# Performance work log

Hardware: AMD Instinct MI355X
Metric: run time of the kernel (lower is better)

## Reference

```python
import jax, jax.numpy as jnp
import numpy as np

CODEBOOK_SIZE = 8192
TOKEN_SIZE = 256
COMMITMENT_COST = 0.25


def setup_inputs() -> dict:
    key = jax.random.key(0)
    k1, k2 = jax.random.split(key)
    z = jax.random.normal(k1, (32, 1024, TOKEN_SIZE), dtype=jnp.float32)
    # embedding initialized uniform in [-1/K, 1/K] as in torch module
    embedding = jax.random.uniform(
        k2, (CODEBOOK_SIZE, TOKEN_SIZE), dtype=jnp.float32,
        minval=-1.0 / CODEBOOK_SIZE, maxval=1.0 / CODEBOOK_SIZE)
    return {"z": z, "embedding": embedding}


def reference(z, embedding):
    B, T, D = z.shape
    zf = z.reshape(B * T, D)                               # [N, D]
    # squared euclidean distances: ||z||^2 + ||e||^2 - 2 z.e
    d = (jnp.sum(zf * zf, axis=1, keepdims=True)
         + jnp.sum(embedding * embedding, axis=1)
         - 2.0 * jnp.einsum('nd,kd->nk', zf, embedding))   # [N, K]
    idx = jnp.argmin(d, axis=1)                            # [N]
    z_q = embedding[idx].reshape(B, T, D)                  # codebook gather
    commitment_loss = COMMITMENT_COST * jnp.mean(
        (jax.lax.stop_gradient(z_q) - z) ** 2)
    codebook_loss = jnp.mean((z_q - jax.lax.stop_gradient(z)) ** 2)
    loss = commitment_loss + codebook_loss                 # ema_update=False
    # straight-through estimator
    z_q_st = z + jax.lax.stop_gradient(z_q - z)
    return (z_q_st, loss, commitment_loss, codebook_loss,
            idx.reshape(B, T))
```

## Files before the change

### kernel.cpp

```cpp
#include <hip/hip_runtime.h>
#include <hip/hip_bf16.h>
#include <cfloat>

#define N_TOK   32768
#define K_CODES 8192
#define D_DIM   256
#define BTOK    128
#define CHUNK   128
#define NSPLIT  4
#define SPLITK  (K_CODES / NSPLIT)
#define CTAU_M  3.0e-5f
#define CAND_MM 2.4e-5f
#define MAXCAND 16
#define RBTOK   32
#define NRS     8
#define RSPLIT  (K_CODES / NRS)

typedef __attribute__((ext_vector_type(4)))  short bf16x4;
typedef __attribute__((ext_vector_type(8)))  short bf16x8;
typedef __attribute__((ext_vector_type(16))) float f32x16;


__device__ __forceinline__ float np_sumsq256(const float* __restrict__ row) {
    #pragma clang fp contract(off)
    float blk[2];
    #pragma unroll
    for (int b = 0; b < 2; b++) {
        const float* x = row + b * 128;
        float r[8];
        #pragma unroll
        for (int j = 0; j < 8; j++) { float v = x[j]; r[j] = v * v; }
        for (int i = 8; i < 128; i += 8) {
            #pragma unroll
            for (int j = 0; j < 8; j++) { float v = x[i + j]; r[j] += v * v; }
        }
        blk[b] = ((r[0] + r[1]) + (r[2] + r[3])) + ((r[4] + r[5]) + (r[6] + r[7]));
    }
    return blk[0] + blk[1];
}

__device__ __forceinline__ float np_einsum256(const float* __restrict__ a,
                                              const float* __restrict__ b) {
    #pragma clang fp contract(off)
    float A0 = 0.f, A1 = 0.f, A2 = 0.f, A3 = 0.f;
    for (int m = 0; m < 256; m += 16) {
        A0 = a[m+ 0]*b[m+ 0] + (a[m+ 4]*b[m+ 4] + (a[m+ 8]*b[m+ 8] + (a[m+12]*b[m+12] + A0)));
        A1 = a[m+ 1]*b[m+ 1] + (a[m+ 5]*b[m+ 5] + (a[m+ 9]*b[m+ 9] + (a[m+13]*b[m+13] + A1)));
        A2 = a[m+ 2]*b[m+ 2] + (a[m+ 6]*b[m+ 6] + (a[m+10]*b[m+10] + (a[m+14]*b[m+14] + A2)));
        A3 = a[m+ 3]*b[m+ 3] + (a[m+ 7]*b[m+ 7] + (a[m+11]*b[m+11] + (a[m+15]*b[m+15] + A3)));
    }
    return (A0 + A1) + (A2 + A3);
}

__device__ __forceinline__ float np_dtilde(float Cn, float e2k, float g) {
    #pragma clang fp contract(off)
    float t = Cn + e2k;
    float d = t - 2.0f * g;
    return d;
}

__device__ __forceinline__ unsigned short bf16_rne(float f) {
    unsigned u = __float_as_uint(f);
    unsigned r = u + 0x7fffu + ((u >> 16) & 1u);
    return (unsigned short)(r >> 16);
}
__device__ __forceinline__ void split_bf16(float f, short& hi, short& lo) {
    unsigned short h = bf16_rne(f);
    hi = (short)h;
    float hf = __uint_as_float(((unsigned)h) << 16);
    lo = (short)bf16_rne(f - hf);
}
__device__ __forceinline__ bf16x8 lo8(bf16x8 h, float4 a, float4 b) {
    float f[8] = {a.x, a.y, a.z, a.w, b.x, b.y, b.z, b.w};
    bf16x8 r;
    #pragma unroll
    for (int i = 0; i < 8; i += 2) {
        float d0 = f[i]     - __uint_as_float(((unsigned)(unsigned short)h[i])     << 16);
        float d1 = f[i + 1] - __uint_as_float(((unsigned)(unsigned short)h[i + 1]) << 16);
        __hip_bfloat162 p = __float22bfloat162_rn(make_float2(d0, d1));
        unsigned u; __builtin_memcpy(&u, &p, 4);
        r[i]     = (short)(u & 0xffffu);
        r[i + 1] = (short)(u >> 16);
    }
    return r;
}

#define MFMA3(A, ah, al, bh, bl) \
    A = __builtin_amdgcn_mfma_f32_32x32x16_bf16(ah, bh, A, 0, 0, 0); \
    A = __builtin_amdgcn_mfma_f32_32x32x16_bf16(ah, bl, A, 0, 0, 0); \
    A = __builtin_amdgcn_mfma_f32_32x32x16_bf16(al, bh, A, 0, 0, 0);

__global__ __launch_bounds__(256) void prep_e_kernel(
    const float* __restrict__ emb, float* __restrict__ e2np,
    float* __restrict__ e2h, unsigned* __restrict__ ccount,
    double* __restrict__ loss_sum)
{
    int k = blockIdx.x * 256 + threadIdx.x;
    float v = np_sumsq256(emb + (size_t)k * D_DIM);
    e2np[k] = v;
    e2h[k]  = 0.5f * v;
    if (k == 0) { *ccount = 0u; *loss_sum = 0.0; }
}

__global__ __launch_bounds__(256) void prep_z_kernel(
    const float* __restrict__ z, float* __restrict__ Cnp)
{
    int t = blockIdx.x * 256 + threadIdx.x;
    Cnp[t] = np_sumsq256(z + (size_t)t * D_DIM);
}

__global__ __launch_bounds__(256) void cvt_e_kernel(
    const float* __restrict__ src, short* __restrict__ hi, short* __restrict__ lo)
{
    size_t p = ((size_t)blockIdx.x * 256 + threadIdx.x) * 8;
    float4 v0 = *(const float4*)(src + p);
    float4 v1 = *(const float4*)(src + p + 4);
    short h[8], l[8];
    split_bf16(v0.x, h[0], l[0]); split_bf16(v0.y, h[1], l[1]);
    split_bf16(v0.z, h[2], l[2]); split_bf16(v0.w, h[3], l[3]);
    split_bf16(v1.x, h[4], l[4]); split_bf16(v1.y, h[5], l[5]);
    split_bf16(v1.z, h[6], l[6]); split_bf16(v1.w, h[7], l[7]);
    bf16x8 vh = {h[0],h[1],h[2],h[3],h[4],h[5],h[6],h[7]};
    bf16x8 vl = {l[0],l[1],l[2],l[3],l[4],l[5],l[6],l[7]};
    *(bf16x8*)(hi + p) = vh;
    *(bf16x8*)(lo + p) = vl;
}

__global__ __launch_bounds__(256) void cvt_zhi_kernel(
    const float* __restrict__ src, short* __restrict__ hi)
{
    size_t p = ((size_t)blockIdx.x * 256 + threadIdx.x) * 8;
    float4 v0 = *(const float4*)(src + p);
    float4 v1 = *(const float4*)(src + p + 4);
    bf16x8 vh = {(short)bf16_rne(v0.x), (short)bf16_rne(v0.y),
                 (short)bf16_rne(v0.z), (short)bf16_rne(v0.w),
                 (short)bf16_rne(v1.x), (short)bf16_rne(v1.y),
                 (short)bf16_rne(v1.z), (short)bf16_rne(v1.w)};
    *(bf16x8*)(hi + p) = vh;
}

#define B_ESH 0
#define B_ESL 4096
#define B_ZSH 8192
#define B_ZSL 12288
#define TILE1 1024

__global__ __launch_bounds__(256, 2) void bulk_kernel(
    const float* __restrict__ zf, const short* __restrict__ zhi,
    const short* __restrict__ ehi, const short* __restrict__ elo,
    const float* __restrict__ e2h,
    float* __restrict__ m1a, float* __restrict__ m2a, int* __restrict__ i1a)
{
    __shared__ __align__(16) short smem[2][16384];
    __shared__ float e2s[2][CHUNK];
    __shared__ float s1m[BTOK], s2m[BTOK];
    __shared__ int   i1m[BTOK];

    const int tid  = threadIdx.x;
    const int lane = tid & 63;
    const int w    = tid >> 6;
    const int wt   = w & 1, wc = w >> 1;
    const int g     = blockIdx.x & 255;
    const int split = blockIdx.x >> 8;
    const int tok0  = g * BTOK;
    const int cs0   = split * SPLITK;

    const int r0 = tid >> 2, q0 = tid & 3;
    const int r1 = r0 + 64;
    const int so0 = r0 * 32 + ((q0 ^ ((r0 >> 1) & 3)) << 3);
    const int so1 = r1 * 32 + ((q0 ^ ((r1 >> 1) & 3)) << 3);

    const int l31 = lane & 31, hh = lane >> 5;
    const int swz = (l31 >> 1) & 3;
    const int arow = (wc * 64 + l31) * 32;
    const int brow = (wt * 64 + l31) * 32;
    const int a0 = arow + ((hh ^ swz) << 3);
    const int a1 = arow + (((2 + hh) ^ swz) << 3);
    const int b0 = brow + ((hh ^ swz) << 3);
    const int b1 = brow + (((2 + hh) ^ swz) << 3);

    float m1[2] = {-FLT_MAX, -FLT_MAX}, m2[2] = {-FLT_MAX, -FLT_MAX};
    int   k1[2] = {0x7fffffff, 0x7fffffff};

    bf16x8 eh0p, el0p, eh1p, el1p, zh0p, zh1p;
    float4 zf0ap, zf0bp, zf1ap, zf1bp;
    float  e2vp = 0.f;

    f32x16 acc[2][2];
    #pragma unroll
    for (int i = 0; i < 2; i++)
        #pragma unroll
        for (int j = 0; j < 2; j++)
            #pragma unroll
            for (int r = 0; r < 16; r++) acc[i][j][r] = 0.f;

    const int NST = (SPLITK / CHUNK) * 8;

    auto ISSUE = [&](int s) {
        const int c  = s >> 3;
        const int st = s & 7;
        const int code0 = cs0 + c * CHUNK;
        const int d0 = st * 32;
        const size_t ei0 = ((size_t)(code0 + r0) << 8) + d0 + (q0 << 3);
        const size_t ei1 = ((size_t)(code0 + r1) << 8) + d0 + (q0 << 3);
        const size_t zi0 = ((size_t)(tok0 + r0) << 8) + d0 + (q0 << 3);
        const size_t zi1 = ((size_t)(tok0 + r1) << 8) + d0 + (q0 << 3);
        eh0p = *(const bf16x8*)(ehi + ei0);
        el0p = *(const bf16x8*)(elo + ei0);
        eh1p = *(const bf16x8*)(ehi + ei1);
        el1p = *(const bf16x8*)(elo + ei1);
        zh0p = *(const bf16x8*)(zhi + zi0);
        zh1p = *(const bf16x8*)(zhi + zi1);
        zf0ap = *(const float4*)(zf + zi0);
        zf0bp = *(const float4*)(zf + zi0 + 4);
        zf1ap = *(const float4*)(zf + zi1);
        zf1bp = *(const float4*)(zf + zi1 + 4);
        if (st == 0 && tid < CHUNK) e2vp = e2h[code0 + tid];
    };

    auto STORE = [&](int buf, int s) {
        bf16x8 zl0 = lo8(zh0p, zf0ap, zf0bp);
        bf16x8 zl1 = lo8(zh1p, zf1ap, zf1bp);
        short* sm = smem[buf];
        *(bf16x8*)(sm + B_ESH + so0) = eh0p;
        *(bf16x8*)(sm + B_ESL + so0) = el0p;
        *(bf16x8*)(sm + B_ESH + so1) = eh1p;
        *(bf16x8*)(sm + B_ESL + so1) = el1p;
        *(bf16x8*)(sm + B_ZSH + so0) = zh0p;
        *(bf16x8*)(sm + B_ZSL + so0) = zl0;
        *(bf16x8*)(sm + B_ZSH + so1) = zh1p;
        *(bf16x8*)(sm + B_ZSL + so1) = zl1;
        if ((s & 7) == 0 && tid < CHUNK) e2s[(s >> 3) & 1][tid] = e2vp;
    };

    ISSUE(0);
    STORE(0, 0);
    __syncthreads();

    #pragma unroll 2
    for (int s = 0; s < NST; s++) {
        const int cur = s & 1;
        if (s + 1 < NST) ISSUE(s + 1);
        {
            const short* sm = smem[cur];
            {
                bf16x8 a0h = *(const bf16x8*)(sm + B_ESH + a0);
                bf16x8 a0l = *(const bf16x8*)(sm + B_ESL + a0);
                bf16x8 a1h = *(const bf16x8*)(sm + B_ESH + TILE1 + a0);
                bf16x8 a1l = *(const bf16x8*)(sm + B_ESL + TILE1 + a0);
                bf16x8 b0h = *(const bf16x8*)(sm + B_ZSH + b0);
                bf16x8 b0l = *(const bf16x8*)(sm + B_ZSL + b0);
                bf16x8 b1h = *(const bf16x8*)(sm + B_ZSH + TILE1 + b0);
                bf16x8 b1l = *(const bf16x8*)(sm + B_ZSL + TILE1 + b0);
                MFMA3(acc[0][0], a0h, a0l, b0h, b0l);
                MFMA3(acc[0][1], a0h, a0l, b1h, b1l);
                MFMA3(acc[1][0], a1h, a1l, b0h, b0l);
                MFMA3(acc[1][1], a1h, a1l, b1h, b1l);
            }
            {
                bf16x8 a0h = *(const bf16x8*)(sm + B_ESH + a1);
                bf16x8 a0l = *(const bf16x8*)(sm + B_ESL + a1);
                bf16x8 a1h = *(const bf16x8*)(sm + B_ESH + TILE1 + a1);
                bf16x8 a1l = *(const bf16x8*)(sm + B_ESL + TILE1 + a1);
                bf16x8 b0h = *(const bf16x8*)(sm + B_ZSH + b1);
                bf16x8 b0l = *(const bf16x8*)(sm + B_ZSL + b1);
                bf16x8 b1h = *(const bf16x8*)(sm + B_ZSH + TILE1 + b1);
                bf16x8 b1l = *(const bf16x8*)(sm + B_ZSL + TILE1 + b1);
                MFMA3(acc[0][0], a0h, a0l, b0h, b0l);
                MFMA3(acc[0][1], a0h, a0l, b1h, b1l);
                MFMA3(acc[1][0], a1h, a1l, b0h, b0l);
                MFMA3(acc[1][1], a1h, a1l, b1h, b1l);
            }
        }
        if ((s & 7) == 7) {
            const int code0 = cs0 + (s >> 3) * CHUNK;
            const float* e2c = e2s[(s >> 3) & 1];
            #pragma unroll
            for (int tc = 0; tc < 2; tc++) {
                float ev[16];
                #pragma unroll
                for (int r = 0; r < 16; r++)
                    ev[r] = e2c[wc * 64 + tc * 32 + hh * 4 + (r & 3) + ((r >> 2) << 3)];
                #pragma unroll
                for (int tt = 0; tt < 2; tt++) {
                    #pragma unroll
                    for (int r = 0; r < 16; r++) {
                        float a = acc[tc][tt][r] - ev[r];
                        int code = code0 + wc * 64 + tc * 32 + hh * 4 + (r & 3) + ((r >> 2) << 3);
                        if (a > m1[tt]) { m2[tt] = m1[tt]; m1[tt] = a; k1[tt] = code; }
                        else if (a > m2[tt]) m2[tt] = a;
                    }
                }
            }
            #pragma unroll
            for (int i = 0; i < 2; i++)
                #pragma unroll
                for (int j = 0; j < 2; j++)
                    #pragma unroll
                    for (int r = 0; r < 16; r++) acc[i][j][r] = 0.f;
        }
        if (s + 1 < NST) STORE(cur ^ 1, s + 1);
        __syncthreads();
    }

    #pragma unroll
    for (int tt = 0; tt < 2; tt++) {
        float o1 = __shfl_xor(m1[tt], 32);
        float o2 = __shfl_xor(m2[tt], 32);
        int   oi = __shfl_xor(k1[tt], 32);
        bool take = (o1 > m1[tt]) || (o1 == m1[tt] && oi < k1[tt]);
        float w1 = take ? o1 : m1[tt];
        int   wi = take ? oi : k1[tt];
        float ls = take ? m1[tt] : o1;
        m2[tt] = fmaxf(fmaxf(m2[tt], o2), ls);
        m1[tt] = w1; k1[tt] = wi;
    }
    __syncthreads();
    if (wc == 0 && lane < 32) {
        #pragma unroll
        for (int tt = 0; tt < 2; tt++) {
            int tl = wt * 64 + tt * 32 + lane;
            s1m[tl] = m1[tt]; s2m[tl] = m2[tt]; i1m[tl] = k1[tt];
        }
    }
    __syncthreads();
    if (wc == 1 && lane < 32) {
        #pragma unroll
        for (int tt = 0; tt < 2; tt++) {
            int tl = wt * 64 + tt * 32 + lane;
            float a1 = s1m[tl], a2 = s2m[tl]; int ai = i1m[tl];
            bool take = (a1 > m1[tt]) || (a1 == m1[tt] && ai < k1[tt]);
            float w1 = take ? a1 : m1[tt];
            int   wi = take ? ai : k1[tt];
            float ls = take ? m1[tt] : a1;
            float w2 = fmaxf(fmaxf(m2[tt], a2), ls);
            size_t t = (size_t)(tok0 + tl) * NSPLIT + split;
            m1a[t] = w1; m2a[t] = w2; i1a[t] = wi;
        }
    }
}

__global__ __launch_bounds__(256) void merge_kernel(
    const float* __restrict__ m1a, const float* __restrict__ m2a,
    const int* __restrict__ i1a, float* __restrict__ m1f,
    int* __restrict__ idxf, int* __restrict__ clist,
    unsigned* __restrict__ ccount, unsigned* __restrict__ ccnt_g)
{
    int t = blockIdx.x * 256 + threadIdx.x;
    ccnt_g[t] = 0u;
    float w1 = m1a[t * NSPLIT], w2 = m2a[t * NSPLIT];
    int   wi = i1a[t * NSPLIT];
    #pragma unroll
    for (int s = 1; s < NSPLIT; s++) {
        float a1 = m1a[t * NSPLIT + s], a2 = m2a[t * NSPLIT + s];
        int   ai = i1a[t * NSPLIT + s];
        bool take = (a1 > w1) || (a1 == w1 && ai < wi);
        float n1 = take ? a1 : w1;
        int   ni = take ? ai : wi;
        float ls = take ? w1 : a1;
        w2 = fmaxf(fmaxf(w2, a2), ls);
        w1 = n1; wi = ni;
    }
    idxf[t] = wi; m1f[t] = w1;
    if (w1 - w2 < CTAU_M) {
        unsigned p = atomicAdd(ccount, 1u);
        clist[p] = t;
    }
}

#define R_ESH 0
#define R_ESL 4096
#define R_ZSH 8192
#define R_ZSL 9216

__global__ __launch_bounds__(256) void rescue_kernel(
    const float* __restrict__ zf, const short* __restrict__ zhi,
    const short* __restrict__ ehi, const short* __restrict__ elo,
    const float* __restrict__ e2h, const float* __restrict__ m1f,
    const unsigned* __restrict__ ccount, const int* __restrict__ clist,
    unsigned* __restrict__ ccnt_g, int* __restrict__ cand_g)
{
    const unsigned count = *ccount;
    const unsigned base  = blockIdx.x * RBTOK;
    if (base >= count) return;
    const int nt = min(RBTOK, (int)(count - base));
    const int sp = blockIdx.y;

    __shared__ __align__(16) short rsm[10240];
    __shared__ int   tls[RBTOK];
    __shared__ float thr[RBTOK];
    __shared__ float e2s[CHUNK];

    const int tid  = threadIdx.x;
    const int lane = tid & 63;
    const int w    = tid >> 6;

    if (tid < RBTOK) {
        int s = (tid < nt) ? tid : (nt - 1);
        int t = clist[base + s];
        tls[tid] = t;
        thr[tid] = (tid < nt) ? (m1f[t] - CAND_MM) : FLT_MAX;
    }
    __syncthreads();

    const int l31 = lane & 31, hh = lane >> 5;
    const float mythr = thr[l31];
    const int   mytok = tls[l31];
    const int swz = (l31 >> 1) & 3;
    const int arow = (w * 32 + l31) * 32;
    const int brow = l31 * 32;
    const int a0 = arow + ((hh ^ swz) << 3);
    const int a1 = arow + (((2 + hh) ^ swz) << 3);
    const int b0 = brow + ((hh ^ swz) << 3);
    const int b1 = brow + (((2 + hh) ^ swz) << 3);

    const int er0 = tid >> 2, eq0 = tid & 3;
    const int er1 = er0 + 64;
    const int eso0 = er0 * 32 + ((eq0 ^ ((er0 >> 1) & 3)) << 3);
    const int eso1 = er1 * 32 + ((eq0 ^ ((er1 >> 1) & 3)) << 3);
    const int zr = (tid & 127) >> 2, zq = tid & 3;
    const int zso = zr * 32 + ((zq ^ ((zr >> 1) & 3)) << 3);

    for (int c = 0; c < RSPLIT / CHUNK; c++) {
        const int code0 = sp * RSPLIT + c * CHUNK;
        const float e2v = (tid < CHUNK) ? e2h[code0 + tid] : 0.f;
        f32x16 acc;
        #pragma unroll
        for (int r = 0; r < 16; r++) acc[r] = 0.f;

        for (int st = 0; st < 8; st++) {
            const int d0 = st * 32;
            const size_t ei0 = ((size_t)(code0 + er0) << 8) + d0 + (eq0 << 3);
            const size_t ei1 = ((size_t)(code0 + er1) << 8) + d0 + (eq0 << 3);
            bf16x8 eh0 = *(const bf16x8*)(ehi + ei0);
            bf16x8 el0 = *(const bf16x8*)(elo + ei0);
            bf16x8 eh1 = *(const bf16x8*)(ehi + ei1);
            bf16x8 el1 = *(const bf16x8*)(elo + ei1);
            bf16x8 zh = {}, zl = {};
            if (tid < 128) {
                const size_t zi = ((size_t)tls[zr] << 8) + d0 + (zq << 3);
                zh = *(const bf16x8*)(zhi + zi);
                float4 za = *(const float4*)(zf + zi);
                float4 zb = *(const float4*)(zf + zi + 4);
                zl = lo8(zh, za, zb);
            }
            __syncthreads();
            *(bf16x8*)(rsm + R_ESH + eso0) = eh0;
            *(bf16x8*)(rsm + R_ESL + eso0) = el0;
            *(bf16x8*)(rsm + R_ESH + eso1) = eh1;
            *(bf16x8*)(rsm + R_ESL + eso1) = el1;
            if (tid < 128) {
                *(bf16x8*)(rsm + R_ZSH + zso) = zh;
                *(bf16x8*)(rsm + R_ZSL + zso) = zl;
            }
            if (st == 0 && tid < CHUNK) e2s[tid] = e2v;
            __syncthreads();
            {
                bf16x8 ah = *(const bf16x8*)(rsm + R_ESH + a0);
                bf16x8 al = *(const bf16x8*)(rsm + R_ESL + a0);
                bf16x8 bh = *(const bf16x8*)(rsm + R_ZSH + b0);
                bf16x8 bl = *(const bf16x8*)(rsm + R_ZSL + b0);
                MFMA3(acc, ah, al, bh, bl);
            }
            {
                bf16x8 ah = *(const bf16x8*)(rsm + R_ESH + a1);
                bf16x8 al = *(const bf16x8*)(rsm + R_ESL + a1);
                bf16x8 bh = *(const bf16x8*)(rsm + R_ZSH + b1);
                bf16x8 bl = *(const bf16x8*)(rsm + R_ZSL + b1);
                MFMA3(acc, ah, al, bh, bl);
            }
        }
        #pragma unroll
        for (int r = 0; r < 16; r++) {
            const int local = w * 32 + hh * 4 + (r & 3) + ((r >> 2) << 3);
            float a = acc[r] - e2s[local];
            if (a >= mythr) {
                unsigned p = atomicAdd(&ccnt_g[mytok], 1u);
                if (p < MAXCAND) cand_g[(size_t)mytok * MAXCAND + p] = code0 + local;
            }
        }
    }
}

__global__ __launch_bounds__(256) void resolve_kernel(
    const float* __restrict__ z, const float* __restrict__ emb,
    const float* __restrict__ e2np, const float* __restrict__ Cnp,
    const unsigned* __restrict__ ccount, const int* __restrict__ clist,
    const unsigned* __restrict__ ccnt_g, const int* __restrict__ cand_g,
    int* __restrict__ idxf)
{
    const unsigned count = *ccount;
    const int lane = threadIdx.x & 63;
    const int w    = threadIdx.x >> 6;
    for (unsigned c = blockIdx.x * 4 + w; c < count; c += gridDim.x * 4) {
        const int t = clist[c];
        const int n = (int)min(ccnt_g[t], (unsigned)MAXCAND);
        float bd = FLT_MAX; int bk = 0x7fffffff;
        if (lane < n) {
            const int k = cand_g[(size_t)t * MAXCAND + lane];
            float g = np_einsum256(z + (size_t)t * D_DIM, emb + (size_t)k * D_DIM);
            bd = np_dtilde(Cnp[t], e2np[k], g);
            bk = k;
        }
        #pragma unroll
        for (int off = 32; off >= 1; off >>= 1) {
            float od = __shfl_xor(bd, off);
            int   ok = __shfl_xor(bk, off);
            if (od < bd || (od == bd && ok < bk)) { bd = od; bk = ok; }
        }
        if (lane == 0 && n > 0) idxf[t] = bk;
    }
}

__global__ __launch_bounds__(256) void out_loss_kernel(
    const float* __restrict__ z, const float* __restrict__ emb,
    const int* __restrict__ idxf, float* __restrict__ out0,
    double* __restrict__ loss_sum)
{
    const int total4 = N_TOK * (D_DIM / 4);
    double lsum = 0.0;
    for (int p = blockIdx.x * 256 + threadIdx.x; p < total4; p += gridDim.x * 256) {
        const int n  = p >> 6;
        const int d4 = p & 63;
        const int k  = idxf[n];
        float4 zv = ((const float4*)z)[p];
        float4 ev = ((const float4*)(emb + (size_t)k * D_DIM))[d4];
        float dx = ev.x - zv.x, dy = ev.y - zv.y,
              dz = ev.z - zv.z, dw = ev.w - zv.w;
        float4 o;
        o.x = zv.x + dx; o.y = zv.y + dy; o.z = zv.z + dz; o.w = zv.w + dw;
        ((float4*)out0)[p] = o;
        lsum += (double)dx * dx + (double)dy * dy
              + (double)dz * dz + (double)dw * dw;
    }
    #pragma unroll
    for (int off = 32; off >= 1; off >>= 1) lsum += __shfl_xor(lsum, off);
    __shared__ double wsum[4];
    const int wv = threadIdx.x >> 6;
    if ((threadIdx.x & 63) == 0) wsum[wv] = lsum;
    __syncthreads();
    if (threadIdx.x == 0)
        atomicAdd(loss_sum, wsum[0] + wsum[1] + wsum[2] + wsum[3]);
}

__global__ __launch_bounds__(256) void finalize_kernel(
    const int* __restrict__ idxf, const double* __restrict__ loss_sum,
    float* __restrict__ out)
{
    const int t = blockIdx.x * 256 + threadIdx.x;
    if (t < N_TOK) out[8388611 + t] = (float)idxf[t];
    if (t == 0) {
        double mse = *loss_sum * (1.0 / 8388608.0);
        out[8388608] = (float)(1.25 * mse);
        out[8388609] = (float)(0.25 * mse);
        out[8388610] = (float)mse;
    }
}

extern "C" void kernel_launch(void* const* d_in, const int* in_sizes, int n_in,
                              void* d_out, int out_size, void* d_ws, size_t ws_size,
                              hipStream_t stream)
{
    const float* z   = (const float*)d_in[0];
    const float* emb = (const float*)d_in[1];
    float* out = (float*)d_out;
    char*  ws  = (char*)d_ws;
    char*  ob  = (char*)d_out;

    short*    ehi    = (short*)(ob + 0);
    short*    elo    = (short*)(ob + 4194304);
    short*    zhi    = (short*)(ob + 8388608);
    float*    m1a    = (float*)(ob + 25165824);
    float*    m2a    = (float*)(ob + 25690112);
    int*      i1a    = (int*)(ob + 26214400);
    int*      cand_g = (int*)(ob + 26738688);

    double*   loss_sum = (double*)(ws + 0);
    unsigned* ccount   = (unsigned*)(ws + 8);
    float*    e2np     = (float*)(ws + 16);
    float*    e2h      = (float*)(ws + 32784);
    float*    Cnp      = (float*)(ws + 65552);
    float*    m1f      = (float*)(ws + 196624);
    int*      idxf     = (int*)(ws + 327696);
    int*      clist    = (int*)(ws + 458768);
    unsigned* ccnt_g   = (unsigned*)(ws + 589840);

    prep_e_kernel<<<dim3(K_CODES / 256), dim3(256), 0, stream>>>(
        emb, e2np, e2h, ccount, loss_sum);
    prep_z_kernel<<<dim3(N_TOK / 256), dim3(256), 0, stream>>>(z, Cnp);
    cvt_e_kernel<<<dim3(K_CODES * D_DIM / 8 / 256), dim3(256), 0, stream>>>(emb, ehi, elo);
    cvt_zhi_kernel<<<dim3(N_TOK * D_DIM / 8 / 256), dim3(256), 0, stream>>>(z, zhi);
    bulk_kernel<<<dim3((N_TOK / BTOK) * NSPLIT), dim3(256), 0, stream>>>(
        z, zhi, ehi, elo, e2h, m1a, m2a, i1a);
    merge_kernel<<<dim3(N_TOK / 256), dim3(256), 0, stream>>>(
        m1a, m2a, i1a, m1f, idxf, clist, ccount, ccnt_g);
    rescue_kernel<<<dim3(N_TOK / RBTOK, NRS), dim3(256), 0, stream>>>(
        z, zhi, ehi, elo, e2h, m1f, ccount, clist, ccnt_g, cand_g);
    resolve_kernel<<<dim3(128), dim3(256), 0, stream>>>(
        z, emb, e2np, Cnp, ccount, clist, ccnt_g, cand_g, idxf);
    out_loss_kernel<<<dim3(1024), dim3(256), 0, stream>>>(
        z, emb, idxf, out, loss_sum);
    finalize_kernel<<<dim3(N_TOK / 256), dim3(256), 0, stream>>>(
        idxf, loss_sum, out);
}
```

Before: 802.0 us.

## Load bf16 tiles directly into LDS via global_load_lds, recompute z hi/lo split

The main distance kernel now copies the embedding hi/lo and z hi bf16 tiles straight from global memory into shared memory with the global_load_lds builtin. Before, they were staged through registers and written with ds_write. The XOR swizzle moves into the global address so each lane's LDS destination stays contiguous. The z low part is now computed from the fp32 z alone by a new split helper, so the zhi register copy is no longer needed. This cuts VGPR pressure and LDS store instructions, but the asynchronous writes go into the other buffer while the current one is read, so correctness depends on the existing barrier and vmcnt ordering.

```diff
diff --git a/kernel.cpp b/kernel.cpp
--- a/kernel.cpp
+++ b/kernel.cpp
@@ -84,6 +84,26 @@
     }
     return r;
 }
+__device__ __forceinline__ uint4 zsplit8(float4 a, float4 b) {
+    float f[8] = {a.x, a.y, a.z, a.w, b.x, b.y, b.z, b.w};
+    unsigned u[4];
+    #pragma unroll
+    for (int i = 0; i < 4; i++) {
+        __hip_bfloat162 hp = __float22bfloat162_rn(make_float2(f[2*i], f[2*i+1]));
+        unsigned hu; __builtin_memcpy(&hu, &hp, 4);
+        float h0 = __uint_as_float(hu << 16);
+        float h1 = __uint_as_float(hu & 0xffff0000u);
+        __hip_bfloat162 lp = __float22bfloat162_rn(make_float2(f[2*i] - h0, f[2*i+1] - h1));
+        __builtin_memcpy(&u[i], &lp, 4);
+    }
+    return make_uint4(u[0], u[1], u[2], u[3]);
+}
+
+__device__ __forceinline__ void gl_lds16(const short* g, short* l) {
+    __builtin_amdgcn_global_load_lds(
+        (const __attribute__((address_space(1))) void*)g,
+        (__attribute__((address_space(3))) void*)l, 16, 0, 0);
+}
 
 #define MFMA3(A, ah, al, bh, bl) \
     A = __builtin_amdgcn_mfma_f32_32x32x16_bf16(ah, bh, A, 0, 0, 0); \
@@ -167,8 +187,12 @@
 
     const int r0 = tid >> 2, q0 = tid & 3;
     const int r1 = r0 + 64;
-    const int so0 = r0 * 32 + ((q0 ^ ((r0 >> 1) & 3)) << 3);
-    const int so1 = r1 * 32 + ((q0 ^ ((r1 >> 1) & 3)) << 3);
+    const int swz0 = (r0 >> 1) & 3;
+    const int qs   = q0 ^ swz0;
+    const int so0 = r0 * 32 + (qs << 3);
+    const int so1 = r1 * 32 + (qs << 3);
+    const int dls0 = w * 512;
+    const int dls1 = w * 512 + 2048;
 
     const int l31 = lane & 31, hh = lane >> 5;
     const int swz = (l31 >> 1) & 3;
@@ -182,7 +206,6 @@
     float m1[2] = {-FLT_MAX, -FLT_MAX}, m2[2] = {-FLT_MAX, -FLT_MAX};
     int   k1[2] = {0x7fffffff, 0x7fffffff};
 
-    bf16x8 eh0p, el0p, eh1p, el1p, zh0p, zh1p;
     float4 zf0ap, zf0bp, zf1ap, zf1bp;
     float  e2vp = 0.f;
 
@@ -196,21 +219,24 @@
 
     const int NST = (SPLITK / CHUNK) * 8;
 
-    auto ISSUE = [&](int s) {
+    auto ISSUE = [&](int s, int buf) {
         const int c  = s >> 3;
         const int st = s & 7;
         const int code0 = cs0 + c * CHUNK;
         const int d0 = st * 32;
-        const size_t ei0 = ((size_t)(code0 + r0) << 8) + d0 + (q0 << 3);
-        const size_t ei1 = ((size_t)(code0 + r1) << 8) + d0 + (q0 << 3);
+        short* sm = smem[buf];
+        const size_t eg0 = ((size_t)(code0 + r0) << 8) + d0 + (qs << 3);
+        const size_t eg1 = ((size_t)(code0 + r1) << 8) + d0 + (qs << 3);
+        const size_t zg0 = ((size_t)(tok0 + r0) << 8) + d0 + (qs << 3);
+        const size_t zg1 = ((size_t)(tok0 + r1) << 8) + d0 + (qs << 3);
+        gl_lds16(ehi + eg0, sm + B_ESH + dls0);
+        gl_lds16(ehi + eg1, sm + B_ESH + dls1);
+        gl_lds16(elo + eg0, sm + B_ESL + dls0);
+        gl_lds16(elo + eg1, sm + B_ESL + dls1);
+        gl_lds16(zhi + zg0, sm + B_ZSH + dls0);
+        gl_lds16(zhi + zg1, sm + B_ZSH + dls1);
         const size_t zi0 = ((size_t)(tok0 + r0) << 8) + d0 + (q0 << 3);
         const size_t zi1 = ((size_t)(tok0 + r1) << 8) + d0 + (q0 << 3);
-        eh0p = *(const bf16x8*)(ehi + ei0);
-        el0p = *(const bf16x8*)(elo + ei0);
-        eh1p = *(const bf16x8*)(ehi + ei1);
-        el1p = *(const bf16x8*)(elo + ei1);
-        zh0p = *(const bf16x8*)(zhi + zi0);
-        zh1p = *(const bf16x8*)(zhi + zi1);
         zf0ap = *(const float4*)(zf + zi0);
         zf0bp = *(const float4*)(zf + zi0 + 4);
         zf1ap = *(const float4*)(zf + zi1);
@@ -219,28 +245,22 @@
     };
 
     auto STORE = [&](int buf, int s) {
-        bf16x8 zl0 = lo8(zh0p, zf0ap, zf0bp);
-        bf16x8 zl1 = lo8(zh1p, zf1ap, zf1bp);
+        uint4 zl0 = zsplit8(zf0ap, zf0bp);
+        uint4 zl1 = zsplit8(zf1ap, zf1bp);
         short* sm = smem[buf];
-        *(bf16x8*)(sm + B_ESH + so0) = eh0p;
-        *(bf16x8*)(sm + B_ESL + so0) = el0p;
-        *(bf16x8*)(sm + B_ESH + so1) = eh1p;
-        *(bf16x8*)(sm + B_ESL + so1) = el1p;
-        *(bf16x8*)(sm + B_ZSH + so0) = zh0p;
-        *(bf16x8*)(sm + B_ZSL + so0) = zl0;
-        *(bf16x8*)(sm + B_ZSH + so1) = zh1p;
-        *(bf16x8*)(sm + B_ZSL + so1) = zl1;
+        *(uint4*)(sm + B_ZSL + so0) = zl0;
+        *(uint4*)(sm + B_ZSL + so1) = zl1;
         if ((s & 7) == 0 && tid < CHUNK) e2s[(s >> 3) & 1][tid] = e2vp;
     };
 
-    ISSUE(0);
+    ISSUE(0, 0);
     STORE(0, 0);
     __syncthreads();
 
     #pragma unroll 2
     for (int s = 0; s < NST; s++) {
         const int cur = s & 1;
-        if (s + 1 < NST) ISSUE(s + 1);
+        if (s + 1 < NST) ISSUE(s + 1, cur ^ 1);
         {
             const short* sm = smem[cur];
             {
```

Result: slower. 859.7 us (+7.2%).

## Split bulk distance kernel across eight waves with smaller per-wave tiles

Applied to the files above, without the earlier changes.

The bulk MFMA kernel moves from 256 to 512 threads per block. Each wave now owns a 32-code by 64-token sub-tile instead of 64 by 64, so it holds half the accumulators, and each thread stages half as many global-to-LDS loads. The cross-wave argmax merge becomes a serialized chain over four code-waves using shared memory with extra barriers. The aim is lower register pressure and more waves in flight to hide memory and LDS latency, at the cost of more LDS traffic per MFMA (B fragments are re-read by more waves) and more synchronisation.

```diff
diff --git a/kernel.cpp b/kernel.cpp
--- a/kernel.cpp
+++ b/kernel.cpp
@@ -145,7 +145,7 @@
 #define B_ZSL 12288
 #define TILE1 1024
 
-__global__ __launch_bounds__(256, 2) void bulk_kernel(
+__global__ __launch_bounds__(512, 4) void bulk_kernel(
     const float* __restrict__ zf, const short* __restrict__ zhi,
     const short* __restrict__ ehi, const short* __restrict__ elo,
     const float* __restrict__ e2h,
@@ -159,20 +159,19 @@
     const int tid  = threadIdx.x;
     const int lane = tid & 63;
     const int w    = tid >> 6;
-    const int wt   = w & 1, wc = w >> 1;
+    const int wt   = w & 1;
+    const int wc   = w >> 1;
     const int g     = blockIdx.x & 255;
     const int split = blockIdx.x >> 8;
     const int tok0  = g * BTOK;
     const int cs0   = split * SPLITK;
 
     const int r0 = tid >> 2, q0 = tid & 3;
-    const int r1 = r0 + 64;
     const int so0 = r0 * 32 + ((q0 ^ ((r0 >> 1) & 3)) << 3);
-    const int so1 = r1 * 32 + ((q0 ^ ((r1 >> 1) & 3)) << 3);
 
     const int l31 = lane & 31, hh = lane >> 5;
     const int swz = (l31 >> 1) & 3;
-    const int arow = (wc * 64 + l31) * 32;
+    const int arow = (wc * 32 + l31) * 32;
     const int brow = (wt * 64 + l31) * 32;
     const int a0 = arow + ((hh ^ swz) << 3);
     const int a1 = arow + (((2 + hh) ^ swz) << 3);
@@ -182,17 +181,15 @@
     float m1[2] = {-FLT_MAX, -FLT_MAX}, m2[2] = {-FLT_MAX, -FLT_MAX};
     int   k1[2] = {0x7fffffff, 0x7fffffff};
 
-    bf16x8 eh0p, el0p, eh1p, el1p, zh0p, zh1p;
-    float4 zf0ap, zf0bp, zf1ap, zf1bp;
+    bf16x8 eh0p, el0p, zh0p;
+    float4 zf0ap, zf0bp;
     float  e2vp = 0.f;
 
-    f32x16 acc[2][2];
-    #pragma unroll
-    for (int i = 0; i < 2; i++)
-        #pragma unroll
-        for (int j = 0; j < 2; j++)
-            #pragma unroll
-            for (int r = 0; r < 16; r++) acc[i][j][r] = 0.f;
+    f32x16 acc[2];
+    #pragma unroll
+    for (int j = 0; j < 2; j++)
+        #pragma unroll
+        for (int r = 0; r < 16; r++) acc[j][r] = 0.f;
 
     const int NST = (SPLITK / CHUNK) * 8;
 
@@ -201,35 +198,23 @@
         const int st = s & 7;
         const int code0 = cs0 + c * CHUNK;
         const int d0 = st * 32;
-        const size_t ei0 = ((size_t)(code0 + r0) << 8) + d0 + (q0 << 3);
-        const size_t ei1 = ((size_t)(code0 + r1) << 8) + d0 + (q0 << 3);
-        const size_t zi0 = ((size_t)(tok0 + r0) << 8) + d0 + (q0 << 3);
-        const size_t zi1 = ((size_t)(tok0 + r1) << 8) + d0 + (q0 << 3);
-        eh0p = *(const bf16x8*)(ehi + ei0);
-        el0p = *(const bf16x8*)(elo + ei0);
-        eh1p = *(const bf16x8*)(ehi + ei1);
-        el1p = *(const bf16x8*)(elo + ei1);
-        zh0p = *(const bf16x8*)(zhi + zi0);
-        zh1p = *(const bf16x8*)(zhi + zi1);
-        zf0ap = *(const float4*)(zf + zi0);
-        zf0bp = *(const float4*)(zf + zi0 + 4);
-        zf1ap = *(const float4*)(zf + zi1);
-        zf1bp = *(const float4*)(zf + zi1 + 4);
+        const size_t ei = ((size_t)(code0 + r0) << 8) + d0 + (q0 << 3);
+        const size_t zi = ((size_t)(tok0 + r0) << 8) + d0 + (q0 << 3);
+        eh0p = *(const bf16x8*)(ehi + ei);
+        el0p = *(const bf16x8*)(elo + ei);
+        zh0p = *(const bf16x8*)(zhi + zi);
+        zf0ap = *(const float4*)(zf + zi);
+        zf0bp = *(const float4*)(zf + zi + 4);
         if (st == 0 && tid < CHUNK) e2vp = e2h[code0 + tid];
     };
 
     auto STORE = [&](int buf, int s) {
         bf16x8 zl0 = lo8(zh0p, zf0ap, zf0bp);
-        bf16x8 zl1 = lo8(zh1p, zf1ap, zf1bp);
         short* sm = smem[buf];
         *(bf16x8*)(sm + B_ESH + so0) = eh0p;
         *(bf16x8*)(sm + B_ESL + so0) = el0p;
-        *(bf16x8*)(sm + B_ESH + so1) = eh1p;
-        *(bf16x8*)(sm + B_ESL + so1) = el1p;
         *(bf16x8*)(sm + B_ZSH + so0) = zh0p;
         *(bf16x8*)(sm + B_ZSL + so0) = zl0;
-        *(bf16x8*)(sm + B_ZSH + so1) = zh1p;
-        *(bf16x8*)(sm + B_ZSL + so1) = zl1;
         if ((s & 7) == 0 && tid < CHUNK) e2s[(s >> 3) & 1][tid] = e2vp;
     };
 
@@ -244,60 +229,47 @@
         {
             const short* sm = smem[cur];
             {
-                bf16x8 a0h = *(const bf16x8*)(sm + B_ESH + a0);
-                bf16x8 a0l = *(const bf16x8*)(sm + B_ESL + a0);
-                bf16x8 a1h = *(const bf16x8*)(sm + B_ESH + TILE1 + a0);
-                bf16x8 a1l = *(const bf16x8*)(sm + B_ESL + TILE1 + a0);
+                bf16x8 ah  = *(const bf16x8*)(sm + B_ESH + a0);
+                bf16x8 al  = *(const bf16x8*)(sm + B_ESL + a0);
                 bf16x8 b0h = *(const bf16x8*)(sm + B_ZSH + b0);
                 bf16x8 b0l = *(const bf16x8*)(sm + B_ZSL + b0);
                 bf16x8 b1h = *(const bf16x8*)(sm + B_ZSH + TILE1 + b0);
                 bf16x8 b1l = *(const bf16x8*)(sm + B_ZSL + TILE1 + b0);
-                MFMA3(acc[0][0], a0h, a0l, b0h, b0l);
-                MFMA3(acc[0][1], a0h, a0l, b1h, b1l);
-                MFMA3(acc[1][0], a1h, a1l, b0h, b0l);
-                MFMA3(acc[1][1], a1h, a1l, b1h, b1l);
+                MFMA3(acc[0], ah, al, b0h, b0l);
+                MFMA3(acc[1], ah, al, b1h, b1l);
             }
             {
-                bf16x8 a0h = *(const bf16x8*)(sm + B_ESH + a1);
-                bf16x8 a0l = *(const bf16x8*)(sm + B_ESL + a1);
-                bf16x8 a1h = *(const bf16x8*)(sm + B_ESH + TILE1 + a1);
-                bf16x8 a1l = *(const bf16x8*)(sm + B_ESL + TILE1 + a1);
+                bf16x8 ah  = *(const bf16x8*)(sm + B_ESH + a1);
+                bf16x8 al  = *(const bf16x8*)(sm + B_ESL + a1);
                 bf16x8 b0h = *(const bf16x8*)(sm + B_ZSH + b1);
                 bf16x8 b0l = *(const bf16x8*)(sm + B_ZSL + b1);
                 bf16x8 b1h = *(const bf16x8*)(sm + B_ZSH + TILE1 + b1);
                 bf16x8 b1l = *(const bf16x8*)(sm + B_ZSL + TILE1 + b1);
-                MFMA3(acc[0][0], a0h, a0l, b0h, b0l);
-                MFMA3(acc[0][1], a0h, a0l, b1h, b1l);
-                MFMA3(acc[1][0], a1h, a1l, b0h, b0l);
-                MFMA3(acc[1][1], a1h, a1l, b1h, b1l);
+                MFMA3(acc[0], ah, al, b0h, b0l);
+                MFMA3(acc[1], ah, al, b1h, b1l);
             }
         }
         if ((s & 7) == 7) {
             const int code0 = cs0 + (s >> 3) * CHUNK;
             const float* e2c = e2s[(s >> 3) & 1];
+            float ev[16];
             #pragma unroll
-            for (int tc = 0; tc < 2; tc++) {
-                float ev[16];
+            for (int r = 0; r < 16; r++)
+                ev[r] = e2c[wc * 32 + hh * 4 + (r & 3) + ((r >> 2) << 3)];
+            #pragma unroll
+            for (int tt = 0; tt < 2; tt++) {
                 #pragma unroll
-                for (int r = 0; r < 16; r++)
-                    ev[r] = e2c[wc * 64 + tc * 32 + hh * 4 + (r & 3) + ((r >> 2) << 3)];
+                for (int r = 0; r < 16; r++) {
+                    float a = acc[tt][r] - ev[r];
+                    int code = code0 + wc * 32 + hh * 4 + (r & 3) + ((r >> 2) << 3);
+                    if (a > m1[tt]) { m2[tt] = m1[tt]; m1[tt] = a; k1[tt] = code; }
+                    else if (a > m2[tt]) m2[tt] = a;
+                }
+            }
+            #pragma unroll
+            for (int j = 0; j < 2; j++)
                 #pragma unroll
-                for (int tt = 0; tt < 2; tt++) {
-                    #pragma unroll
-                    for (int r = 0; r < 16; r++) {
-                        float a = acc[tc][tt][r] - ev[r];
-                        int code = code0 + wc * 64 + tc * 32 + hh * 4 + (r & 3) + ((r >> 2) << 3);
-                        if (a > m1[tt]) { m2[tt] = m1[tt]; m1[tt] = a; k1[tt] = code; }
-                        else if (a > m2[tt]) m2[tt] = a;
-                    }
-                }
-            }
-            #pragma unroll
-            for (int i = 0; i < 2; i++)
-                #pragma unroll
-                for (int j = 0; j < 2; j++)
-                    #pragma unroll
-                    for (int r = 0; r < 16; r++) acc[i][j][r] = 0.f;
+                for (int r = 0; r < 16; r++) acc[j][r] = 0.f;
         }
         if (s + 1 < NST) STORE(cur ^ 1, s + 1);
         __syncthreads();
@@ -324,7 +296,24 @@
         }
     }
     __syncthreads();
-    if (wc == 1 && lane < 32) {
+    #pragma unroll
+    for (int mw = 1; mw < 3; mw++) {
+        if (wc == mw && lane < 32) {
+            #pragma unroll
+            for (int tt = 0; tt < 2; tt++) {
+                int tl = wt * 64 + tt * 32 + lane;
+                float a1 = s1m[tl], a2 = s2m[tl]; int ai = i1m[tl];
+                bool take = (a1 > m1[tt]) || (a1 == m1[tt] && ai < k1[tt]);
+                float w1 = take ? a1 : m1[tt];
+                int   wi = take ? ai : k1[tt];
+                float ls = take ? m1[tt] : a1;
+                float w2 = fmaxf(fmaxf(m2[tt], a2), ls);
+                s1m[tl] = w1; s2m[tl] = w2; i1m[tl] = wi;
+            }
+        }
+        __syncthreads();
+    }
+    if (wc == 3 && lane < 32) {
         #pragma unroll
         for (int tt = 0; tt < 2; tt++) {
             int tl = wt * 64 + tt * 32 + lane;
@@ -590,7 +579,7 @@
     prep_z_kernel<<<dim3(N_TOK / 256), dim3(256), 0, stream>>>(z, Cnp);
     cvt_e_kernel<<<dim3(K_CODES * D_DIM / 8 / 256), dim3(256), 0, stream>>>(emb, ehi, elo);
     cvt_zhi_kernel<<<dim3(N_TOK * D_DIM / 8 / 256), dim3(256), 0, stream>>>(z, zhi);
-    bulk_kernel<<<dim3((N_TOK / BTOK) * NSPLIT), dim3(256), 0, stream>>>(
+    bulk_kernel<<<dim3((N_TOK / BTOK) * NSPLIT), dim3(512), 0, stream>>>(
         z, zhi, ehi, elo, e2h, m1a, m2a, i1a);
     merge_kernel<<<dim3(N_TOK / 256), dim3(256), 0, stream>>>(
         m1a, m2a, i1a, m1f, idxf, clist, ccount, ccnt_g);
```

New measurement: 808.4 us. About the same (+0.8%).
